# Kernel tuning notes

Hardware: AMD Instinct MI355X
Metric: run time of the kernel (lower is better)

## Reference

```python
import jax, jax.numpy as jnp
import numpy as np

# ---- config (matches init_kwargs: seek_thermal, K=1024 points, P=5 persons) ----
H, W = 150, 200
N = H * W
K = 1024          # max_num_points
P = 5             # max_num_persons
HFOV_DEG, VFOV_DEG = 81.0, 59.0
DEPTH_MIN = 3.0   # valid depth threshold
BIG = 1e9         # sentinel for invalid depths when sorting


def _camera_rays():
    fx = W / (2.0 * np.tan(np.deg2rad(HFOV_DEG) / 2.0))
    fy = H / (2.0 * np.tan(np.deg2rad(VFOV_DEG) / 2.0))
    x, y = np.meshgrid(np.arange(W, dtype=np.float32), np.arange(H, dtype=np.float32), indexing='xy')
    x_cam = (x - W / 2.0) / fx   # (H, W)
    y_cam = (y - H / 2.0) / fy   # (H, W)
    return jnp.asarray(x_cam), jnp.asarray(y_cam)


def _masked_quantile(d_sorted, n, q):
    # linear-interpolation quantile over the first n sorted entries (torch.quantile default)
    pos = q * jnp.maximum(n.astype(d_sorted.dtype) - 1.0, 0.0)          # (B, P)
    lo = jnp.floor(pos).astype(jnp.int32)
    hi = jnp.ceil(pos).astype(jnp.int32)
    frac = pos - lo.astype(d_sorted.dtype)
    vlo = jnp.take_along_axis(d_sorted, lo[..., None], axis=-1)[..., 0]
    vhi = jnp.take_along_axis(d_sorted, hi[..., None], axis=-1)[..., 0]
    return vlo + (vhi - vlo) * frac


def setup_inputs() -> dict:
    key = jax.random.key(0)
    k1, k2, k3 = jax.random.split(key, 3)
    B = 128
    depth = jax.random.uniform(k1, (B, H, W), dtype=jnp.float32) * 8.0            # depths 0..8m
    indicator = jax.random.randint(k2, (B, H, W), 0, P + 1).astype(jnp.float32)   # person ids 0..P
    extra = jax.random.normal(k3, (B, H, W), dtype=jnp.float32)                   # unused channel
    depth_mask_3C = jnp.stack([depth, indicator, extra], axis=1)                  # (B, 3, H, W)
    return {"depth_mask_3C": depth_mask_3C}


def reference(depth_mask_3C) -> jnp.ndarray:
    B = depth_mask_3C.shape[0]
    dtype = depth_mask_3C.dtype
    x_cam, y_cam = _camera_rays()

    depth = depth_mask_3C[:, 0].reshape(B, N)                         # (B, N)
    indicator = jnp.round(depth_mask_3C[:, 1]).reshape(B, N)          # (B, N)

    # per-person membership masks, persons 1..P
    pids = jnp.arange(1, P + 1, dtype=dtype)
    mask = indicator[:, None, :] == pids[None, :, None]               # (B, P, N)
    valid = mask & (depth[:, None, :] > DEPTH_MIN)                    # (B, P, N)

    # grouped IQR outlier bounds via masked sort + interpolated quantile
    d = jnp.where(valid, depth[:, None, :], BIG)
    d_sorted = jnp.sort(d, axis=-1)                                   # (B, P, N)
    n_valid = valid.sum(axis=-1)                                      # (B, P)
    q1 = _masked_quantile(d_sorted, n_valid, 0.25)
    q3 = _masked_quantile(d_sorted, n_valid, 0.75)
    iqr = q3 - q1
    lb = (q1 - 1.5 * iqr)[..., None]
    ub = (q3 + 1.5 * iqr)[..., None]
    keep = valid & (depth[:, None, :] >= lb) & (depth[:, None, :] <= ub)   # (B, P, N)

    # 3D points: (x_cam*z, y_cam*z, z) per pixel
    rays = jnp.stack([x_cam.reshape(N), y_cam.reshape(N), jnp.ones((N,), dtype)], axis=-1)  # (N, 3)
    pts = depth[..., None] * rays[None]                               # (B, N, 3)

    # deterministic variant of sampling: take the first K kept points in raster order
    rank = jnp.cumsum(keep.astype(jnp.int32), axis=-1) - 1            # (B, P, N)
    idx = jnp.where(keep & (rank < K), rank, K)                       # overflow/invalid -> slot K (discarded)

    def fill(idx_p, pts_b):                                           # idx_p (N,), pts_b (N, 3)
        return jnp.zeros((K + 1, 3), dtype).at[idx_p].set(pts_b)[:K]

    buf = jax.vmap(lambda i_b, p_b: jax.vmap(fill, in_axes=(0, None))(i_b, p_b))(idx, pts)  # (B, P, K, 3)

    # presence flag goes into slot K, channel 0
    flag = (keep.sum(axis=-1) > 0).astype(dtype)                      # (B, P)
    extra = flag[..., None, None] * jnp.array([1.0, 0.0, 0.0], dtype) # (B, P, 1, 3)
    seg = jnp.concatenate([buf, extra], axis=2)                       # (B, P, K+1, 3)
    return jnp.transpose(seg, (0, 3, 1, 2)).reshape(B, 3, P * (K + 1))
```

## Files before the change

### kernel.cpp

```cpp
#include <hip/hip_runtime.h>
#include <math.h>

#define HGT 150
#define WID 200
#define NPIX 30000
#define NF4  7500
#define KMAX 1024
#define PMAX 5
#define THREADS 512
#define NWAVES 8
#define CAPW 512
#define CAP  (NWAVES*CAPW)
#define NWORDS 938
#define NWPAD 940
#define NBIN 1024
#define SHIFT 14
#define KBASE 0x40400000u
#define GCAP 128
#define STRIDE_C (PMAX*(KMAX+1))

__device__ __forceinline__ uint32_t wave_incl_scan(uint32_t x, int lane) {
#pragma unroll
    for (int off = 1; off < 64; off <<= 1) {
        uint32_t y = __shfl_up(x, (unsigned)off, 64);
        if (lane >= off) x += y;
    }
    return x;
}
__device__ __forceinline__ uint32_t wave_red_add(uint32_t x) {
#pragma unroll
    for (int off = 32; off >= 1; off >>= 1) x += __shfl_xor(x, off, 64);
    return x;
}
__device__ __forceinline__ uint32_t key_bin(uint32_t key) {
    uint32_t d = (key - KBASE) >> SHIFT;
    return d < NBIN ? d : (NBIN - 1);
}

__device__ void locate_ranks(const uint32_t* hh, int seg, const uint32_t* s_rank,
                             uint32_t* s_tbin, uint32_t* s_tbel, uint32_t* s_ws) {
    const int tid = threadIdx.x, lane = tid & 63, wv = tid >> 6;
    const uint32_t* mine = hh + tid * seg;
    uint32_t segsum = 0;
    for (int j = 0; j < seg; ++j) segsum += mine[j];
    uint32_t inc = wave_incl_scan(segsum, lane);
    if (lane == 63) s_ws[wv] = inc;
    __syncthreads();
    uint32_t tbase = inc - segsum;
    for (int w = 0; w < wv; ++w) tbase += s_ws[w];
#pragma unroll
    for (int k = 0; k < 4; ++k) {
        uint32_t r = s_rank[k];
        if (r >= tbase && r < tbase + segsum) {
            uint32_t c = tbase;
            for (int j = 0; j < seg; ++j) {
                uint32_t h = mine[j];
                if (r < c + h) { s_tbin[k] = (uint32_t)(tid * seg + j); s_tbel[k] = c; break; }
                c += h;
            }
        }
    }
    __syncthreads();
}

__global__ __launch_bounds__(THREADS, 6) void fused(const float* __restrict__ in,
                                                    float* __restrict__ out, int B) {
    const int nbp = B * PMAX;
    int x = blockIdx.x, b, p;
    if ((nbp & 7) == 0) {
        int per = nbp >> 3;
        int slot = (x & 7) * per + (x >> 3);
        b = slot / PMAX; p = slot - b * PMAX;
    } else { b = x / PMAX; p = x - b * PMAX; }

    const float pid = (float)(p + 1);
    const float4* __restrict__ depth4 = (const float4*)(in + (size_t)b * 3 * NPIX);
    const float4* __restrict__ ind4   = depth4 + NF4;
    const int tid = threadIdx.x, lane = tid & 63, wv = tid >> 6;

    __shared__ uint32_t keys[CAP];
    __shared__ unsigned short sidx[CAP];
    __shared__ uint32_t hist[NBIN];
    __shared__ uint32_t vb2[NWPAD];
    __shared__ unsigned short wpfx[NWPAD];
    __shared__ float xc_tab[WID];
    __shared__ float yc_tab[HGT];
    __shared__ uint32_t gbuf[4 * GCAP];
    __shared__ uint32_t gcnt[4];
    __shared__ uint32_t s_ws[NWAVES];
    __shared__ uint32_t s_wcnt[NWAVES];
    __shared__ uint32_t s_rank[4], s_res[4], s_tbin[4], s_tbel[4], s_u[4], s_val[4];
    __shared__ int s_slot[4], s_desc[4];
    __shared__ uint32_t s_dprefix, s_dr;

    for (int i = tid; i < NBIN; i += THREADS) hist[i] = 0;
    {
        const double fxd = (double)WID / (2.0 * tan((81.0 * M_PI / 180.0) * 0.5));
        const double fyd = (double)HGT / (2.0 * tan((59.0 * M_PI / 180.0) * 0.5));
        for (int i = tid; i < WID; i += THREADS) xc_tab[i] = (float)(((double)i - (double)WID / 2.0) / fxd);
        for (int i = tid; i < HGT; i += THREADS) yc_tab[i] = (float)(((double)i - (double)HGT / 2.0) / fyd);
    }
    __syncthreads();

    const uint32_t segbase = (uint32_t)wv * CAPW;
    const uint32_t seglim = segbase + CAPW;
    uint32_t run = 0;
#pragma unroll
    for (int g = 0; g < 5; ++g) {
        float4 dv[3];
        uint32_t nib[3];
        uint32_t cnt_t = 0;
#pragma unroll
        for (int t = 0; t < 3; ++t) {
            int f = (g * 3 + t) * THREADS + tid;
            nib[t] = 0;
            if (f < NF4) {
                dv[t] = depth4[f];
                float4 i4 = ind4[f];
                const float* dd = (const float*)&dv[t];
                const float* ii = (const float*)&i4;
#pragma unroll
                for (int j = 0; j < 4; ++j)
                    if (rintf(ii[j]) == pid && dd[j] > 3.0f) nib[t] |= 1u << j;
                cnt_t += (uint32_t)__popc(nib[t]);
            }
        }
        uint32_t incl = wave_incl_scan(cnt_t, lane);
        uint32_t wtot = __shfl(incl, 63, 64);
        uint32_t pos = segbase + run + incl - cnt_t;
        run += wtot;
#pragma unroll
        for (int t = 0; t < 3; ++t) {
            if (nib[t]) {
                int f = (g * 3 + t) * THREADS + tid;
                const float* dd = (const float*)&dv[t];
#pragma unroll
                for (int j = 0; j < 4; ++j)
                    if ((nib[t] >> j) & 1u) {
                        uint32_t key = __float_as_uint(dd[j]);
                        atomicAdd(&hist[key_bin(key)], 1u);
                        if (pos < seglim) {
                            keys[pos] = key;
                            sidx[pos] = (unsigned short)(f * 4 + j);
                        }
                        ++pos;
                    }
            }
        }
    }
    if (lane == 0) s_wcnt[wv] = run;
    __syncthreads();

    uint32_t n = 0;
    bool over = false;
#pragma unroll
    for (int w = 0; w < NWAVES; ++w) {
        uint32_t c = s_wcnt[w];
        n += c;
        over |= (c > CAPW);
    }

    float* outB = out + (size_t)b * 3 * STRIDE_C + p * (KMAX + 1);

    if (n == 0) {
        for (int r = tid; r <= KMAX; r += THREADS) {
            outB[r] = 0.f; outB[STRIDE_C + r] = 0.f; outB[2 * STRIDE_C + r] = 0.f;
        }
        return;
    }

    uint32_t rank[4]; float posf[2];
    {
        float nf = (float)n;
        posf[0] = 0.25f * fmaxf(nf - 1.0f, 0.0f);
        posf[1] = 0.75f * fmaxf(nf - 1.0f, 0.0f);
        rank[0] = (uint32_t)floorf(posf[0]); rank[1] = (uint32_t)ceilf(posf[0]);
        rank[2] = (uint32_t)floorf(posf[1]); rank[3] = (uint32_t)ceilf(posf[1]);
    }

    if (over) {
        uint32_t v[4];
        for (int k = 0; k < 4; ++k) {
            if (tid == 0) { s_dprefix = 0; s_dr = rank[k]; }
            __syncthreads();
            for (int bit = 30; bit >= 0; --bit) {
                uint32_t pfx = s_dprefix;
                uint32_t c = 0;
                for (int kk = 0; kk < 15; ++kk) {
                    int f = kk * THREADS + tid;
                    if (f < NF4) {
                        float4 d4 = depth4[f]; float4 i4 = ind4[f];
                        const float* dd = (const float*)&d4;
                        const float* ii = (const float*)&i4;
#pragma unroll
                        for (int j = 0; j < 4; ++j)
                            if (rintf(ii[j]) == pid && dd[j] > 3.0f) {
                                uint32_t key = __float_as_uint(dd[j]);
                                if ((key >> (bit + 1)) == pfx && !((key >> bit) & 1u)) ++c;
                            }
                    }
                }
                c = wave_red_add(c);
                if (lane == 0) s_ws[wv] = c;
                __syncthreads();
                uint32_t c0 = 0;
                for (int w = 0; w < NWAVES; ++w) c0 += s_ws[w];
                if (tid == 0) {
                    if (s_dr < c0) s_dprefix = pfx << 1;
                    else { s_dprefix = (pfx << 1) | 1u; s_dr -= c0; }
                }
                __syncthreads();
            }
            v[k] = s_dprefix;
            __syncthreads();
        }
        float f1 = posf[0] - floorf(posf[0]);
        float f3 = posf[1] - floorf(posf[1]);
        float q1 = __uint_as_float(v[0]) + (__uint_as_float(v[1]) - __uint_as_float(v[0])) * f1;
        float q3 = __uint_as_float(v[2]) + (__uint_as_float(v[3]) - __uint_as_float(v[2])) * f3;
        float iqr = q3 - q1;
        float lb = q1 - 1.5f * iqr, ub = q3 + 1.5f * iqr;
        if (tid == 0) {
            const float* depth = (const float*)depth4;
            const float* ind = (const float*)ind4;
            uint32_t r = 0;
            for (int i = 0; i < NPIX; ++i) {
                float d = depth[i];
                if (rintf(ind[i]) == pid && d > 3.0f && d >= lb && d <= ub) {
                    if (r < KMAX) {
                        int row = i / WID, col = i - row * WID;
                        outB[r] = xc_tab[col] * d;
                        outB[STRIDE_C + r] = yc_tab[row] * d;
                        outB[2 * STRIDE_C + r] = d;
                    }
                    ++r;
                }
            }
            s_dr = r;
        }
        __syncthreads();
        uint32_t count = s_dr;
        uint32_t start = count < KMAX ? count : KMAX;
        for (uint32_t r = start + tid; r < KMAX; r += THREADS) {
            outB[r] = 0.f; outB[STRIDE_C + r] = 0.f; outB[2 * STRIDE_C + r] = 0.f;
        }
        if (tid == 0) {
            outB[KMAX] = (count > 0) ? 1.0f : 0.0f;
            outB[STRIDE_C + KMAX] = 0.f; outB[2 * STRIDE_C + KMAX] = 0.f;
        }
        return;
    }

    const uint32_t wn = s_wcnt[wv];

    if (tid == 0) {
#pragma unroll
        for (int k = 0; k < 4; ++k) s_rank[k] = rank[k];
    }
    __syncthreads();
    locate_ranks(hist, NBIN / THREADS, s_rank, s_tbin, s_tbel, s_ws);

    if (tid == 0) {
        uint32_t uq[4]; int nu = 0;
#pragma unroll
        for (int k = 0; k < 4; ++k) {
            s_res[k] = rank[k] - s_tbel[k];
            int fnd = -1;
            for (int u = 0; u < nu; ++u) if (uq[u] == s_tbin[k]) fnd = u;
            if (fnd < 0) { uq[nu] = s_tbin[k]; fnd = nu; ++nu; }
            s_slot[k] = fnd;
        }
#pragma unroll
        for (int u = 0; u < 4; ++u) { s_u[u] = 0xFFFFFFFFu; gcnt[u] = 0; }
        for (int u = 0; u < nu; ++u) if (hist[uq[u]] <= GCAP) s_u[u] = uq[u];
#pragma unroll
        for (int k = 0; k < 4; ++k) s_desc[k] = (hist[uq[s_slot[k]]] > GCAP) ? 1 : 0;
    }
    __syncthreads();

    for (uint32_t i = segbase + lane; i < segbase + wn; i += 64) {
        uint32_t key = keys[i];
        uint32_t bin = key_bin(key);
#pragma unroll
        for (int u = 0; u < 4; ++u)
            if (bin == s_u[u]) {
                uint32_t slot = atomicAdd(&gcnt[u], 1u);
                if (slot < GCAP) gbuf[u * GCAP + slot] = key;
            }
    }
    __syncthreads();
    if (wv < 4) {
        if (!s_desc[wv]) {
            int u = s_slot[wv];
            uint32_t c = gcnt[u];
            uint32_t res = s_res[wv];
            for (uint32_t i = lane; i < c; i += 64) {
                uint32_t xk = gbuf[u * GCAP + i];
                uint32_t less = 0, eq = 0;
                for (uint32_t j = 0; j < c; ++j) {
                    uint32_t y = gbuf[u * GCAP + j];
                    less += (y < xk); eq += (y == xk);
                }
                if (res >= less && res < less + eq) s_val[wv] = xk;
            }
        }
    } else {
        for (int i = (wv - 4) * 64 + lane; i < NWPAD; i += 256) vb2[i] = 0;
    }
    __syncthreads();
    for (int k = 0; k < 4; ++k) if (s_desc[k]) {
        if (tid == 0) { s_dprefix = 0; s_dr = rank[k]; }
        __syncthreads();
        for (int bit = 30; bit >= 0; --bit) {
            uint32_t pfx = s_dprefix;
            uint32_t c = 0;
            for (uint32_t i = segbase + lane; i < segbase + wn; i += 64) {
                uint32_t key = keys[i];
                if ((key >> (bit + 1)) == pfx && !((key >> bit) & 1u)) ++c;
            }
            c = wave_red_add(c);
            if (lane == 0) s_ws[wv] = c;
            __syncthreads();
            uint32_t c0 = 0;
            for (int w = 0; w < NWAVES; ++w) c0 += s_ws[w];
            if (tid == 0) {
                if (s_dr < c0) s_dprefix = pfx << 1;
                else { s_dprefix = (pfx << 1) | 1u; s_dr -= c0; }
            }
            __syncthreads();
        }
        if (tid == 0) s_val[k] = s_dprefix;
        __syncthreads();
    }

    float lb, ub;
    {
        float f1 = posf[0] - floorf(posf[0]);
        float f3 = posf[1] - floorf(posf[1]);
        float v0 = __uint_as_float(s_val[0]), v1 = __uint_as_float(s_val[1]);
        float v2 = __uint_as_float(s_val[2]), v3 = __uint_as_float(s_val[3]);
        float q1 = v0 + (v1 - v0) * f1;
        float q3 = v2 + (v3 - v2) * f3;
        float iqr = q3 - q1;
        lb = q1 - 1.5f * iqr;
        ub = q3 + 1.5f * iqr;
    }

    for (uint32_t i = segbase + lane; i < segbase + wn; i += 64) {
        float d = __uint_as_float(keys[i]);
        if (d >= lb && d <= ub) {
            uint32_t s = sidx[i];
            atomicOr(&vb2[s >> 5], 1u << (s & 31));
        }
    }
    __syncthreads();
    {
        uint4 v4 = make_uint4(0, 0, 0, 0);
        if (tid < NWPAD / 4) v4 = ((const uint4*)vb2)[tid];
        uint32_t pc0 = (uint32_t)__popc(v4.x), pc1 = (uint32_t)__popc(v4.y);
        uint32_t pc2 = (uint32_t)__popc(v4.z), pc3 = (uint32_t)__popc(v4.w);
        uint32_t lsum = pc0 + pc1 + pc2 + pc3;
        uint32_t inc = wave_incl_scan(lsum, lane);
        if (lane == 63) s_ws[wv] = inc;
        __syncthreads();
        uint32_t rn = inc - lsum;
        for (int w = 0; w < wv; ++w) rn += s_ws[w];
        if (tid < NWPAD / 4) {
            ushort4 w4;
            w4.x = (unsigned short)rn;            rn += pc0;
            w4.y = (unsigned short)rn;            rn += pc1;
            w4.z = (unsigned short)rn;            rn += pc2;
            w4.w = (unsigned short)rn;
            ((ushort4*)wpfx)[tid] = w4;
        }
    }
    __syncthreads();
    uint32_t total = 0;
    for (int w = 0; w < NWAVES; ++w) total += s_ws[w];

    for (uint32_t i = segbase + lane; i < segbase + wn; i += 64) {
        uint32_t key = keys[i];
        float d = __uint_as_float(key);
        if (d >= lb && d <= ub) {
            uint32_t s = sidx[i];
            uint32_t w = s >> 5;
            uint32_t base = wpfx[w];
            if (base < KMAX) {
                uint32_t r = base + (uint32_t)__popc(vb2[w] & ((1u << (s & 31)) - 1u));
                if (r < KMAX) {
                    uint32_t row = s / WID;
                    uint32_t col = s - row * WID;
                    outB[r] = xc_tab[col] * d;
                    outB[STRIDE_C + r] = yc_tab[row] * d;
                    outB[2 * STRIDE_C + r] = d;
                }
            }
        }
    }
    uint32_t start = total < KMAX ? total : KMAX;
    for (uint32_t r = start + tid; r < KMAX; r += THREADS) {
        outB[r] = 0.f; outB[STRIDE_C + r] = 0.f; outB[2 * STRIDE_C + r] = 0.f;
    }
    if (tid == 0) {
        outB[KMAX] = (total > 0) ? 1.0f : 0.0f;
        outB[STRIDE_C + KMAX] = 0.f;
        outB[2 * STRIDE_C + KMAX] = 0.f;
    }
}

extern "C" void kernel_launch(void* const* d_in, const int* in_sizes, int n_in,
                              void* d_out, int out_size, void* d_ws, size_t ws_size,
                              hipStream_t stream) {
    (void)n_in; (void)out_size; (void)d_ws; (void)ws_size;
    const float* in = (const float*)d_in[0];
    float* out = (float*)d_out;
    const int B = in_sizes[0] / (3 * NPIX);
    fused<<<B * PMAX, THREADS, 0, stream>>>(in, out, B);
}
```

Before: 98.94 us.

## Assign contiguous pixel ranges per wave and compact with ballot instead of bitmap

```diff
diff --git a/kernel.cpp b/kernel.cpp
--- a/kernel.cpp
+++ b/kernel.cpp
@@ -11,8 +11,6 @@
 #define NWAVES 8
 #define CAPW 512
 #define CAP  (NWAVES*CAPW)
-#define NWORDS 938
-#define NWPAD 940
 #define NBIN 1024
 #define SHIFT 14
 #define KBASE 0x40400000u
@@ -81,8 +79,6 @@
     __shared__ uint32_t keys[CAP];
     __shared__ unsigned short sidx[CAP];
     __shared__ uint32_t hist[NBIN];
-    __shared__ uint32_t vb2[NWPAD];
-    __shared__ unsigned short wpfx[NWPAD];
     __shared__ float xc_tab[WID];
     __shared__ float yc_tab[HGT];
     __shared__ uint32_t gbuf[4 * GCAP];
@@ -104,17 +100,17 @@
 
     const uint32_t segbase = (uint32_t)wv * CAPW;
     const uint32_t seglim = segbase + CAPW;
+    const int fstart = (wv * NF4) / NWAVES;
+    const int fend = ((wv + 1) * NF4) / NWAVES;
     uint32_t run = 0;
-#pragma unroll
-    for (int g = 0; g < 5; ++g) {
+    for (int fb = fstart; fb < fend; fb += 192) {
         float4 dv[3];
         uint32_t nib[3];
-        uint32_t cnt_t = 0;
 #pragma unroll
         for (int t = 0; t < 3; ++t) {
-            int f = (g * 3 + t) * THREADS + tid;
+            int f = fb + t * 64 + lane;
             nib[t] = 0;
-            if (f < NF4) {
+            if (f < fend) {
                 dv[t] = depth4[f];
                 float4 i4 = ind4[f];
                 const float* dd = (const float*)&dv[t];
@@ -122,17 +118,17 @@
 #pragma unroll
                 for (int j = 0; j < 4; ++j)
                     if (rintf(ii[j]) == pid && dd[j] > 3.0f) nib[t] |= 1u << j;
-                cnt_t += (uint32_t)__popc(nib[t]);
-            }
-        }
-        uint32_t incl = wave_incl_scan(cnt_t, lane);
-        uint32_t wtot = __shfl(incl, 63, 64);
-        uint32_t pos = segbase + run + incl - cnt_t;
-        run += wtot;
+            }
+        }
 #pragma unroll
         for (int t = 0; t < 3; ++t) {
+            uint32_t cnt_t = (uint32_t)__popc(nib[t]);
+            uint32_t incl = wave_incl_scan(cnt_t, lane);
+            uint32_t wtot = __shfl(incl, 63, 64);
+            uint32_t pos = segbase + run + incl - cnt_t;
+            run += wtot;
             if (nib[t]) {
-                int f = (g * 3 + t) * THREADS + tid;
+                int f = fb + t * 64 + lane;
                 const float* dd = (const float*)&dv[t];
 #pragma unroll
                 for (int j = 0; j < 4; ++j)
@@ -289,23 +285,19 @@
             }
     }
     __syncthreads();
-    if (wv < 4) {
-        if (!s_desc[wv]) {
-            int u = s_slot[wv];
-            uint32_t c = gcnt[u];
-            uint32_t res = s_res[wv];
-            for (uint32_t i = lane; i < c; i += 64) {
-                uint32_t xk = gbuf[u * GCAP + i];
-                uint32_t less = 0, eq = 0;
-                for (uint32_t j = 0; j < c; ++j) {
-                    uint32_t y = gbuf[u * GCAP + j];
-                    less += (y < xk); eq += (y == xk);
-                }
-                if (res >= less && res < less + eq) s_val[wv] = xk;
-            }
-        }
-    } else {
-        for (int i = (wv - 4) * 64 + lane; i < NWPAD; i += 256) vb2[i] = 0;
+    if (wv < 4 && !s_desc[wv]) {
+        int u = s_slot[wv];
+        uint32_t c = gcnt[u];
+        uint32_t res = s_res[wv];
+        for (uint32_t i = lane; i < c; i += 64) {
+            uint32_t xk = gbuf[u * GCAP + i];
+            uint32_t less = 0, eq = 0;
+            for (uint32_t j = 0; j < c; ++j) {
+                uint32_t y = gbuf[u * GCAP + j];
+                less += (y < xk); eq += (y == xk);
+            }
+            if (res >= less && res < less + eq) s_val[wv] = xk;
+        }
     }
     __syncthreads();
     for (int k = 0; k < 4; ++k) if (s_desc[k]) {
@@ -346,47 +338,37 @@
         ub = q3 + 1.5f * iqr;
     }
 
-    for (uint32_t i = segbase + lane; i < segbase + wn; i += 64) {
-        float d = __uint_as_float(keys[i]);
-        if (d >= lb && d <= ub) {
-            uint32_t s = sidx[i];
-            atomicOr(&vb2[s >> 5], 1u << (s & 31));
-        }
-    }
-    __syncthreads();
     {
-        uint4 v4 = make_uint4(0, 0, 0, 0);
-        if (tid < NWPAD / 4) v4 = ((const uint4*)vb2)[tid];
-        uint32_t pc0 = (uint32_t)__popc(v4.x), pc1 = (uint32_t)__popc(v4.y);
-        uint32_t pc2 = (uint32_t)__popc(v4.z), pc3 = (uint32_t)__popc(v4.w);
-        uint32_t lsum = pc0 + pc1 + pc2 + pc3;
-        uint32_t inc = wave_incl_scan(lsum, lane);
-        if (lane == 63) s_ws[wv] = inc;
-        __syncthreads();
-        uint32_t rn = inc - lsum;
-        for (int w = 0; w < wv; ++w) rn += s_ws[w];
-        if (tid < NWPAD / 4) {
-            ushort4 w4;
-            w4.x = (unsigned short)rn;            rn += pc0;
-            w4.y = (unsigned short)rn;            rn += pc1;
-            w4.z = (unsigned short)rn;            rn += pc2;
-            w4.w = (unsigned short)rn;
-            ((ushort4*)wpfx)[tid] = w4;
-        }
-    }
-    __syncthreads();
-    uint32_t total = 0;
-    for (int w = 0; w < NWAVES; ++w) total += s_ws[w];
-
-    for (uint32_t i = segbase + lane; i < segbase + wn; i += 64) {
-        uint32_t key = keys[i];
-        float d = __uint_as_float(key);
-        if (d >= lb && d <= ub) {
-            uint32_t s = sidx[i];
-            uint32_t w = s >> 5;
-            uint32_t base = wpfx[w];
-            if (base < KMAX) {
-                uint32_t r = base + (uint32_t)__popc(vb2[w] & ((1u << (s & 31)) - 1u));
+        uint32_t kc = 0;
+        for (uint32_t i = segbase + lane; i < segbase + wn; i += 64) {
+            float d = __uint_as_float(keys[i]);
+            kc += (d >= lb && d <= ub) ? 1u : 0u;
+        }
+        kc = wave_red_add(kc);
+        if (lane == 0) s_ws[wv] = kc;
+    }
+    __syncthreads();
+    uint32_t base = 0, total = 0;
+#pragma unroll
+    for (int w = 0; w < NWAVES; ++w) {
+        uint32_t c = s_ws[w];
+        if (w < wv) base += c;
+        total += c;
+    }
+
+    if (base < KMAX) {
+        for (uint32_t i0 = segbase; i0 < segbase + wn; i0 += 64) {
+            uint32_t i = i0 + lane;
+            bool kept = false; float d = 0.f; uint32_t s = 0;
+            if (i < segbase + wn) {
+                uint32_t key = keys[i];
+                d = __uint_as_float(key);
+                kept = (d >= lb && d <= ub);
+                s = sidx[i];
+            }
+            unsigned long long m = __ballot(kept);
+            if (kept) {
+                uint32_t r = base + (uint32_t)__popcll(m & ((1ull << lane) - 1ull));
                 if (r < KMAX) {
                     uint32_t row = s / WID;
                     uint32_t col = s - row * WID;
@@ -395,6 +377,8 @@
                     outB[2 * STRIDE_C + r] = d;
                 }
             }
+            base += (uint32_t)__popcll(m);
+            if (base >= KMAX) break;
         }
     }
     uint32_t start = total < KMAX ? total : KMAX;
```

After: 105.2 us. +6.3%, slower.
